# Kernel optimization log

Hardware: AMD Instinct MI355X
Metric: run time of the kernel (lower is better)

## Reference

```python
import jax, jax.numpy as jnp
import numpy as np
from jax import lax

B, C_IN, C_OUT, H, W = 2, 128, 256, 128, 128
KH = KW = 3
K = KH * KW  # 9 kernel sampling locations
EPS = 1e-5


def setup_inputs() -> dict:
    ks = jax.random.split(jax.random.key(0), 9)
    x = jax.random.normal(ks[0], (B, C_IN, H, W), dtype=jnp.float32)
    # offset/mask conv: 27 = 3*K output channels, 3x3 kernel, stride 1, same pad
    w_off = jax.random.normal(ks[1], (3 * K, C_IN, KH, KW), dtype=jnp.float32) * 0.01
    b_off = jnp.zeros((3 * K,), dtype=jnp.float32)
    # deformable conv weight [C_out, C_in, 3, 3] + bias
    w_dcn = jax.random.normal(ks[2], (C_OUT, C_IN, KH, KW), dtype=jnp.float32) * (1.0 / np.sqrt(C_IN * K))
    b_dcn = jax.random.normal(ks[3], (C_OUT,), dtype=jnp.float32) * 0.01
    # BatchNorm (inference-mode) params
    gamma = 1.0 + 0.1 * jax.random.normal(ks[4], (C_OUT,), dtype=jnp.float32)
    beta = 0.1 * jax.random.normal(ks[5], (C_OUT,), dtype=jnp.float32)
    moving_mean = 0.1 * jax.random.normal(ks[6], (C_OUT,), dtype=jnp.float32)
    moving_var = jax.random.uniform(ks[7], (C_OUT,), dtype=jnp.float32, minval=0.5, maxval=1.5)
    return {"x": x, "w_off": w_off, "b_off": b_off, "w_dcn": w_dcn, "b_dcn": b_dcn,
            "gamma": gamma, "beta": beta, "moving_mean": moving_mean, "moving_var": moving_var}


def _conv2d_nchw(x, w, b):
    y = lax.conv_general_dilated(x, w, window_strides=(1, 1), padding='SAME',
                                 dimension_numbers=('NCHW', 'OIHW', 'NCHW'))
    return y + b[None, :, None, None]


def _bilinear_gather(x, yi, xi):
    """Gather x[b,:,yi,xi] with zero padding outside. x:[B,C,H,W]; yi,xi:[B,K,H,W] int."""
    valid = ((yi >= 0) & (yi < H) & (xi >= 0) & (xi < W)).astype(x.dtype)  # [B,K,H,W]
    yc = jnp.clip(yi, 0, H - 1)
    xc = jnp.clip(xi, 0, W - 1)
    idx = (yc * W + xc).reshape(B, -1)  # [B, K*H*W]
    xf = x.reshape(B, C_IN, H * W)
    g = jax.vmap(lambda xb, ib: xb[:, ib])(xf, idx)  # [B, C, K*H*W]
    return g.reshape(B, C_IN, K, H, W) * valid[:, None]


def _deform_conv(x, offset, mask, w, b):
    """DCNv2 modulated deformable conv, 3x3, stride 1, SAME (pad=1).
    offset: [B, 2K, H, W] with (dy, dx) interleaved per kernel location (tfa/DCNv2 layout).
    mask:   [B, K, H, W] (already sigmoided).
    """
    dy = offset[:, 0::2]  # [B,K,H,W]
    dx = offset[:, 1::2]
    ky = (jnp.arange(K, dtype=jnp.float32) // KW) - 1.0  # kernel y offsets in {-1,0,1}
    kx = (jnp.arange(K, dtype=jnp.float32) % KW) - 1.0
    ii = jnp.arange(H, dtype=jnp.float32)[:, None]
    jj = jnp.arange(W, dtype=jnp.float32)[None, :]
    py = ii[None, None] + ky[None, :, None, None] + dy  # [B,K,H,W] sampling y
    px = jj[None, None] + kx[None, :, None, None] + dx  # [B,K,H,W] sampling x

    y0f = jnp.floor(py)
    x0f = jnp.floor(px)
    wy = (py - y0f)[:, None]  # [B,1,K,H,W]
    wx = (px - x0f)[:, None]
    y0 = y0f.astype(jnp.int32)
    x0 = x0f.astype(jnp.int32)

    v00 = _bilinear_gather(x, y0, x0)
    v01 = _bilinear_gather(x, y0, x0 + 1)
    v10 = _bilinear_gather(x, y0 + 1, x0)
    v11 = _bilinear_gather(x, y0 + 1, x0 + 1)
    val = (v00 * (1 - wy) * (1 - wx) + v01 * (1 - wy) * wx
           + v10 * wy * (1 - wx) + v11 * wy * wx)  # [B,C,K,H,W]
    val = val * mask[:, None]  # modulation

    w_r = w.reshape(C_OUT, C_IN, K)
    out = jnp.einsum('bckhw,ock->bohw', val, w_r)
    return out + b[None, :, None, None]


def reference(x, w_off, b_off, w_dcn, b_dcn, gamma, beta, moving_mean, moving_var):
    weight_info = _conv2d_nchw(x, w_off, b_off)  # [B, 27, H, W]
    o1, o2, m = jnp.split(weight_info, 3, axis=1)
    offset = jnp.concatenate((o1, o2), axis=1)  # [B, 18, H, W]
    mask = jax.nn.sigmoid(m)  # [B, 9, H, W]
    y = _deform_conv(x, offset, mask, w_dcn, b_dcn)
    # BatchNorm2d (inference, channels_first) + ReLU
    inv = gamma / jnp.sqrt(moving_var + EPS)
    y = (y - moving_mean[None, :, None, None]) * inv[None, :, None, None] + beta[None, :, None, None]
    return jax.nn.relu(y)
```

## Files before the change

### kernel.cpp

```cpp
#include <hip/hip_runtime.h>
#include <hip/hip_fp16.h>

#define HH 128
#define WW 128
#define CIN 128
#define COUT 256
#define K9 9
#define HW (HH*WW)
#define PIX (2*HW)
#define KDIM (CIN*K9)
#define BN_EPS 1e-5f

typedef __attribute__((ext_vector_type(8))) short short8;
typedef __attribute__((ext_vector_type(4))) float f32x4;
typedef _Float16 half8 __attribute__((ext_vector_type(8)));
typedef unsigned short u16;
typedef unsigned int u32;

union H8 { short8 s; __half2 h2[4]; half8 h; };

struct __align__(16) Meta16 { ushort4 idx; __half2 w01, w23; };
static_assert(sizeof(Meta16) == 16, "");

__device__ __forceinline__ u16 f2h(float f) {
    union { __half h; u16 u; } x; x.h = __float2half_rn(f); return x.u;
}

__global__ __launch_bounds__(256) void prep_xt(const float* __restrict__ x,
                                               u16* __restrict__ xt) {
    __shared__ float tile[32][129];
    const int b   = blockIdx.y;
    const int hw0 = blockIdx.x * 32;
    const float* __restrict__ xb = x + (size_t)b * (CIN*HW);
    #pragma unroll
    for (int i = 0; i < 16; ++i) {
        const int idx = threadIdx.x + i*256;
        const int c = idx >> 5, hwl = idx & 31;
        tile[hwl][c] = xb[(size_t)c*HW + hw0 + hwl];
    }
    __syncthreads();
    const int hwl = threadIdx.x >> 3;
    const int c0  = (threadIdx.x & 7) * 16;
    short8 s0, s1;
    #pragma unroll
    for (int j = 0; j < 8; ++j) {
        s0[j] = (short)f2h(tile[hwl][c0 + j]);
        s1[j] = (short)f2h(tile[hwl][c0 + 8 + j]);
    }
    u16* dst = xt + ((size_t)b*HW + hw0 + hwl)*CIN + c0;
    *(short8*)dst = s0;
    *(short8*)(dst + 8) = s1;
}

__global__ __launch_bounds__(128) void prep_wall(const float* __restrict__ w_dcn,
                                                 const float* __restrict__ w_off,
                                                 u16* __restrict__ wT2,
                                                 u16* __restrict__ wOffT2) {
    const int c = threadIdx.x;
    const int k = blockIdx.x;
    const int o = blockIdx.y;
    const int s = c >> 5, ch = c & 31;
    const int tt = k*4 + s;
    if (o < COUT) {
        wT2[((size_t)tt*COUT + o)*32 + ch] = f2h(w_dcn[(size_t)o*KDIM + c*K9 + k]);
    } else {
        const int j = o - COUT;
        wOffT2[((size_t)tt*32 + j)*32 + ch] =
            (j < 27) ? f2h(w_off[(size_t)j*KDIM + c*K9 + k]) : (u16)0;
    }
}

__global__ __launch_bounds__(512, 4) __attribute__((amdgpu_waves_per_eu(4, 4)))
void dcn_fused(
    const u16* __restrict__ xt, const u16* __restrict__ wT2,
    const u16* __restrict__ wOffT2, const float* __restrict__ b_off,
    const float* __restrict__ b_dcn, const float* __restrict__ gamma,
    const float* __restrict__ beta, const float* __restrict__ mmean,
    const float* __restrict__ mvar, float* __restrict__ out)
{
    __shared__ __align__(16) u16 Vs[2][64*128];
    __shared__ __align__(16) Meta16 metaL[K9*64];
    float* wiL = (float*)&Vs[0][0];

    const int t = threadIdx.x, l = t & 63, wv = t >> 6;
    const int l15 = l & 15, lq = l >> 4;
    const int bid = (blockIdx.x & 7) * 64 + (blockIdx.x >> 3);
    const int pg0 = bid * 64;
    const int b   = pg0 >> 14;
    const int hw0 = pg0 & 16383;
    const u16* __restrict__ xtb = xt + (size_t)b * (HW*CIN);

    {
        const int pxg = wv >> 1;
        const int jh  = wv & 1;
        const int px  = pxg*16 + l15;
        const int pg  = pg0 + px;
        const int hw  = pg & 16383;
        const int h = hw >> 7, w = hw & 127;
        f32x4 oa = {0.f,0.f,0.f,0.f};
        #pragma unroll
        for (int tt = 0; tt < 36; ++tt) {
            const int k = tt >> 2, c0 = (tt & 3) * 32;
            const int yy = h + (k/3) - 1, xx = w + (k%3) - 1;
            const bool valid = ((unsigned)yy < HH) && ((unsigned)xx < WW);
            const int idx = min(max(yy,0),HH-1)*WW + min(max(xx,0),WW-1);
            H8 bv, av;
            bv.s = *(const short8*)(xtb + (size_t)idx*CIN + c0 + lq*8);
            av.s = *(const short8*)(wOffT2 + ((size_t)tt*32 + jh*16 + l15)*32 + lq*8);
            if (!valid) bv.s = (short8){0,0,0,0,0,0,0,0};
            oa = __builtin_amdgcn_mfma_f32_16x16x32_f16(av.h, bv.h, oa, 0,0,0);
        }
        #pragma unroll
        for (int r = 0; r < 4; ++r)
            wiL[px*33 + jh*16 + lq*4 + r] = oa[r];
        __syncthreads();

        #pragma unroll
        for (int rd = 0; rd < 2; ++rd) {
            const int u = t + rd*512;
            if (u < 576) {
                const int px2 = u & 63, k = u >> 6;
                const int hwp = (pg0 + px2) & 16383;
                const int hp = hwp >> 7, wp = hwp & 127;
                const float dy = wiL[px2*33 + 2*k]     + b_off[2*k];
                const float dx = wiL[px2*33 + 2*k + 1] + b_off[2*k+1];
                const float mm = wiL[px2*33 + 18 + k]  + b_off[18+k];
                const float py = (float)hp + (float)(k/3) - 1.0f + dy;
                const float px_ = (float)wp + (float)(k%3) - 1.0f + dx;
                const float msk = 1.0f / (1.0f + expf(-mm));
                const float y0f = floorf(py), x0f = floorf(px_);
                const float wy = py - y0f, wx = px_ - x0f;
                const int y0 = (int)y0f, x0 = (int)x0f;
                const int y1 = y0 + 1,   x1 = x0 + 1;
                const bool v00 = ((unsigned)y0 < HH) && ((unsigned)x0 < WW);
                const bool v01 = ((unsigned)y0 < HH) && ((unsigned)x1 < WW);
                const bool v10 = ((unsigned)y1 < HH) && ((unsigned)x0 < WW);
                const bool v11 = ((unsigned)y1 < HH) && ((unsigned)x1 < WW);
                const int y0c = min(max(y0,0),HH-1), y1c = min(max(y1,0),HH-1);
                const int x0c = min(max(x0,0),WW-1), x1c = min(max(x1,0),WW-1);
                Meta16 mo;
                mo.idx.x = (u16)(y0c*WW + x0c);
                mo.idx.y = (u16)(y0c*WW + x1c);
                mo.idx.z = (u16)(y1c*WW + x0c);
                mo.idx.w = (u16)(y1c*WW + x1c);
                const float f00 = v00 ? (1.f-wy)*(1.f-wx)*msk : 0.f;
                const float f01 = v01 ? (1.f-wy)*wx*msk       : 0.f;
                const float f10 = v10 ? wy*(1.f-wx)*msk       : 0.f;
                const float f11 = v11 ? wy*wx*msk             : 0.f;
                mo.w01 = __floats2half2_rn(f00, f01);
                mo.w23 = __floats2half2_rn(f10, f11);
                metaL[k*64 + px2] = mo;
            }
        }
        __syncthreads();
    }

    const int pxl  = t >> 3;
    const int cb   = t & 7;
    const int px15 = pxl & 15;

    f32x4 acc[8];
    #pragma unroll
    for (int i = 0; i < 8; ++i) acc[i] = (f32x4){0.f,0.f,0.f,0.f};

    const u16 *g0, *g1, *g2, *g3;
    __half2 wb0, wb1, wb2, wb3;

#define SETMETA(k_) do { \
    const Meta16 mt_ = metaL[(k_)*64 + pxl]; \
    g0 = xtb + (size_t)mt_.idx.x*CIN + cb*8; \
    g1 = xtb + (size_t)mt_.idx.y*CIN + cb*8; \
    g2 = xtb + (size_t)mt_.idx.z*CIN + cb*8; \
    g3 = xtb + (size_t)mt_.idx.w*CIN + cb*8; \
    wb0 = __half2half2(__low2half(mt_.w01)); \
    wb1 = __half2half2(__high2half(mt_.w01)); \
    wb2 = __half2half2(__low2half(mt_.w23)); \
    wb3 = __half2half2(__high2half(mt_.w23)); \
} while (0)

#define ISSUE(cr_, u_) do { \
    cr_[0].s = *(const short8*)(g0 + (u_)*64); \
    cr_[1].s = *(const short8*)(g1 + (u_)*64); \
    cr_[2].s = *(const short8*)(g2 + (u_)*64); \
    cr_[3].s = *(const short8*)(g3 + (u_)*64); \
} while (0)

#define COMBINE_WRITE(cr_, u_, buf_) do { \
    H8 r_; \
    _Pragma("unroll") \
    for (int i_ = 0; i_ < 4; ++i_) \
        r_.h2[i_] = __hfma2(cr_[3].h2[i_], wb3, __hfma2(cr_[2].h2[i_], wb2, \
                    __hfma2(cr_[1].h2[i_], wb1, __hmul2(cr_[0].h2[i_], wb0)))); \
    *(short8*)&Vs[buf_][pxl*128 + ((cb + (u_)*8) ^ px15)*8] = r_.s; \
} while (0)

    H8 cA[4], cB[4];
    SETMETA(0);
    ISSUE(cA, 0); ISSUE(cB, 1);
    COMBINE_WRITE(cA, 0, 0); COMBINE_WRITE(cB, 1, 0);
    __syncthreads();

    int cur = 0;
    for (int k = 0; k < 9; ++k) {
        const bool pf = (k < 8);
        H8 av[4][2];
        #pragma unroll
        for (int s = 0; s < 4; ++s)
            #pragma unroll
            for (int m = 0; m < 2; ++m)
                av[s][m].s = *(const short8*)
                    (wT2 + ((size_t)(k*4 + s)*COUT + wv*32 + m*16 + l15)*32 + lq*8);
        __builtin_amdgcn_sched_barrier(0);
        if (pf) { SETMETA(k+1); ISSUE(cA, 0); ISSUE(cB, 1); }
        __builtin_amdgcn_sched_barrier(0);

        #pragma unroll
        for (int s = 0; s < 4; ++s) {
            #pragma unroll
            for (int nh = 0; nh < 2; ++nh) {
                H8 bf[2];
                #pragma unroll
                for (int j = 0; j < 2; ++j) {
                    const int n = nh*2 + j;
                    bf[j].s = *(const short8*)
                        &Vs[cur][(n*16 + l15)*128 + ((s*4 + lq) ^ l15)*8];
                }
                #pragma unroll
                for (int m = 0; m < 2; ++m)
                    #pragma unroll
                    for (int j = 0; j < 2; ++j)
                        acc[m*4 + nh*2 + j] =
                            __builtin_amdgcn_mfma_f32_16x16x32_f16(
                                av[s][m].h, bf[j].h, acc[m*4 + nh*2 + j], 0, 0, 0);
            }
        }
        if (pf) { COMBINE_WRITE(cA, 0, cur ^ 1); COMBINE_WRITE(cB, 1, cur ^ 1); }
        __syncthreads();
        cur ^= 1;
    }
#undef SETMETA
#undef ISSUE
#undef COMBINE_WRITE

    #pragma unroll
    for (int m = 0; m < 2; ++m) {
        #pragma unroll
        for (int r = 0; r < 4; ++r) {
            const int o = wv*32 + m*16 + lq*4 + r;
            const float sc = gamma[o] * rsqrtf(mvar[o] + BN_EPS);
            const float sh = (b_dcn[o] - mmean[o]) * sc + beta[o];
            float* __restrict__ op = out + ((size_t)(b*COUT + o) << 14) + hw0;
            #pragma unroll
            for (int n = 0; n < 4; ++n) {
                const float v = fmaf(acc[m*4 + n][r], sc, sh);
                op[n*16 + l15] = fmaxf(v, 0.f);
            }
        }
    }
}

extern "C" void kernel_launch(void* const* d_in, const int* in_sizes, int n_in,
                              void* d_out, int out_size, void* d_ws, size_t ws_size,
                              hipStream_t stream) {
    (void)in_sizes; (void)n_in; (void)out_size; (void)ws_size;
    const float* x      = (const float*)d_in[0];
    const float* w_off  = (const float*)d_in[1];
    const float* b_off  = (const float*)d_in[2];
    const float* w_dcn  = (const float*)d_in[3];
    const float* b_dcn  = (const float*)d_in[4];
    const float* gamma  = (const float*)d_in[5];
    const float* beta   = (const float*)d_in[6];
    const float* mmean  = (const float*)d_in[7];
    const float* mvar   = (const float*)d_in[8];
    float* out = (float*)d_out;

    char* ws = (char*)d_ws;
    u16* xtp    = (u16*)ws;
    u16* wT2    = (u16*)(ws + 8388608);
    u16* wOffT2 = (u16*)(ws + 8388608 + 589824);

    prep_xt  <<<dim3(HW/32, 2), 256, 0, stream>>>(x, xtp);
    prep_wall<<<dim3(9, 288), 128, 0, stream>>>(w_dcn, w_off, wT2, wOffT2);
    dcn_fused<<<dim3(PIX/64), 512, 0, stream>>>(xtp, wT2, wOffT2, b_off, b_dcn,
                                                gamma, beta, mmean, mvar, out);
}
```

Measured before the change: 73.39 us.

## Merge prep kernels and split offset-conv K loop across waves

The two preprocessing kernels (input transpose to fp16 NHWC and weight repacking) become one launch that picks its role from the block index, removing a kernel launch and the gap between launches. In the fused kernel the offset/mask conv now splits the 36-step reduction into two halves across wave groups. Each wave computes both 16-row output halves from a single B-operand load, and the two partial sums are stored in separate LDS planes and added when offsets are decoded. This halves the serial MFMA chain per wave and reuses the gathered input, at the cost of an extra LDS plane read per value.

```diff
diff --git a/kernel.cpp b/kernel.cpp
--- a/kernel.cpp
+++ b/kernel.cpp
@@ -26,47 +26,49 @@
     union { __half h; u16 u; } x; x.h = __float2half_rn(f); return x.u;
 }
 
-__global__ __launch_bounds__(256) void prep_xt(const float* __restrict__ x,
-                                               u16* __restrict__ xt) {
+__global__ __launch_bounds__(256) void prep_all(
+    const float* __restrict__ x, const float* __restrict__ w_dcn,
+    const float* __restrict__ w_off, u16* __restrict__ xt,
+    u16* __restrict__ wT2, u16* __restrict__ wOffT2)
+{
     __shared__ float tile[32][129];
-    const int b   = blockIdx.y;
-    const int hw0 = blockIdx.x * 32;
-    const float* __restrict__ xb = x + (size_t)b * (CIN*HW);
-    #pragma unroll
-    for (int i = 0; i < 16; ++i) {
-        const int idx = threadIdx.x + i*256;
-        const int c = idx >> 5, hwl = idx & 31;
-        tile[hwl][c] = xb[(size_t)c*HW + hw0 + hwl];
-    }
-    __syncthreads();
-    const int hwl = threadIdx.x >> 3;
-    const int c0  = (threadIdx.x & 7) * 16;
-    short8 s0, s1;
-    #pragma unroll
-    for (int j = 0; j < 8; ++j) {
-        s0[j] = (short)f2h(tile[hwl][c0 + j]);
-        s1[j] = (short)f2h(tile[hwl][c0 + 8 + j]);
-    }
-    u16* dst = xt + ((size_t)b*HW + hw0 + hwl)*CIN + c0;
-    *(short8*)dst = s0;
-    *(short8*)(dst + 8) = s1;
-}
-
-__global__ __launch_bounds__(128) void prep_wall(const float* __restrict__ w_dcn,
-                                                 const float* __restrict__ w_off,
-                                                 u16* __restrict__ wT2,
-                                                 u16* __restrict__ wOffT2) {
-    const int c = threadIdx.x;
-    const int k = blockIdx.x;
-    const int o = blockIdx.y;
-    const int s = c >> 5, ch = c & 31;
-    const int tt = k*4 + s;
-    if (o < COUT) {
-        wT2[((size_t)tt*COUT + o)*32 + ch] = f2h(w_dcn[(size_t)o*KDIM + c*K9 + k]);
+    if (blockIdx.x < 1024) {
+        const int b   = blockIdx.x >> 9;
+        const int hw0 = (blockIdx.x & 511) * 32;
+        const float* __restrict__ xb = x + (size_t)b * (CIN*HW);
+        #pragma unroll
+        for (int i = 0; i < 16; ++i) {
+            const int idx = threadIdx.x + i*256;
+            const int c = idx >> 5, hwl = idx & 31;
+            tile[hwl][c] = xb[(size_t)c*HW + hw0 + hwl];
+        }
+        __syncthreads();
+        const int hwl = threadIdx.x >> 3;
+        const int c0  = (threadIdx.x & 7) * 16;
+        short8 s0, s1;
+        #pragma unroll
+        for (int j = 0; j < 8; ++j) {
+            s0[j] = (short)f2h(tile[hwl][c0 + j]);
+            s1[j] = (short)f2h(tile[hwl][c0 + 8 + j]);
+        }
+        u16* dst = xt + ((size_t)b*HW + hw0 + hwl)*CIN + c0;
+        *(short8*)dst = s0;
+        *(short8*)(dst + 8) = s1;
     } else {
-        const int j = o - COUT;
-        wOffT2[((size_t)tt*32 + j)*32 + ch] =
-            (j < 27) ? f2h(w_off[(size_t)j*KDIM + c*K9 + k]) : (u16)0;
+        const int u2 = (blockIdx.x - 1024) * 2 + (threadIdx.x >> 7);
+        const int c  = threadIdx.x & 127;
+        const int k  = u2 % 9;
+        const int o  = u2 / 9;
+        const int s = c >> 5, ch = c & 31;
+        const int tt = k*4 + s;
+        if (o < COUT) {
+            wT2[((size_t)tt*COUT + o)*32 + ch] =
+                f2h(w_dcn[(size_t)o*KDIM + c*K9 + k]);
+        } else {
+            const int j = o - COUT;
+            wOffT2[((size_t)tt*32 + j)*32 + ch] =
+                (j < 27) ? f2h(w_off[(size_t)j*KDIM + c*K9 + k]) : (u16)0;
+        }
     }
 }
 
@@ -80,7 +82,6 @@
 {
     __shared__ __align__(16) u16 Vs[2][64*128];
     __shared__ __align__(16) Meta16 metaL[K9*64];
-    float* wiL = (float*)&Vs[0][0];
 
     const int t = threadIdx.x, l = t & 63, wv = t >> 6;
     const int l15 = l & 15, lq = l >> 4;
@@ -91,30 +92,38 @@
     const u16* __restrict__ xtb = xt + (size_t)b * (HW*CIN);
 
     {
-        const int pxg = wv >> 1;
-        const int jh  = wv & 1;
+        const int pxg = wv & 3;
+        const int ks  = wv >> 2;
         const int px  = pxg*16 + l15;
         const int pg  = pg0 + px;
         const int hw  = pg & 16383;
         const int h = hw >> 7, w = hw & 127;
-        f32x4 oa = {0.f,0.f,0.f,0.f};
-        #pragma unroll
-        for (int tt = 0; tt < 36; ++tt) {
+        f32x4 oa0 = {0.f,0.f,0.f,0.f}, oa1 = {0.f,0.f,0.f,0.f};
+        #pragma unroll
+        for (int it = 0; it < 18; ++it) {
+            const int tt = ks*18 + it;
             const int k = tt >> 2, c0 = (tt & 3) * 32;
             const int yy = h + (k/3) - 1, xx = w + (k%3) - 1;
             const bool valid = ((unsigned)yy < HH) && ((unsigned)xx < WW);
             const int idx = min(max(yy,0),HH-1)*WW + min(max(xx,0),WW-1);
-            H8 bv, av;
+            H8 bv, a0, a1;
             bv.s = *(const short8*)(xtb + (size_t)idx*CIN + c0 + lq*8);
-            av.s = *(const short8*)(wOffT2 + ((size_t)tt*32 + jh*16 + l15)*32 + lq*8);
+            a0.s = *(const short8*)(wOffT2 + ((size_t)tt*32 + l15)*32      + lq*8);
+            a1.s = *(const short8*)(wOffT2 + ((size_t)tt*32 + 16 + l15)*32 + lq*8);
             if (!valid) bv.s = (short8){0,0,0,0,0,0,0,0};
-            oa = __builtin_amdgcn_mfma_f32_16x16x32_f16(av.h, bv.h, oa, 0,0,0);
-        }
-        #pragma unroll
-        for (int r = 0; r < 4; ++r)
-            wiL[px*33 + jh*16 + lq*4 + r] = oa[r];
-        __syncthreads();
-
+            oa0 = __builtin_amdgcn_mfma_f32_16x16x32_f16(a0.h, bv.h, oa0, 0,0,0);
+            oa1 = __builtin_amdgcn_mfma_f32_16x16x32_f16(a1.h, bv.h, oa1, 0,0,0);
+        }
+        float* plane = (float*)&Vs[ks][0];
+        #pragma unroll
+        for (int r = 0; r < 4; ++r) {
+            plane[px*33 + lq*4 + r]      = oa0[r];
+            plane[px*33 + 16 + lq*4 + r] = oa1[r];
+        }
+        __syncthreads();
+
+        const float* __restrict__ p0 = (const float*)&Vs[0][0];
+        const float* __restrict__ p1 = (const float*)&Vs[1][0];
         #pragma unroll
         for (int rd = 0; rd < 2; ++rd) {
             const int u = t + rd*512;
@@ -122,9 +131,9 @@
                 const int px2 = u & 63, k = u >> 6;
                 const int hwp = (pg0 + px2) & 16383;
                 const int hp = hwp >> 7, wp = hwp & 127;
-                const float dy = wiL[px2*33 + 2*k]     + b_off[2*k];
-                const float dx = wiL[px2*33 + 2*k + 1] + b_off[2*k+1];
-                const float mm = wiL[px2*33 + 18 + k]  + b_off[18+k];
+                const float dy = p0[px2*33 + 2*k]     + p1[px2*33 + 2*k]     + b_off[2*k];
+                const float dx = p0[px2*33 + 2*k + 1] + p1[px2*33 + 2*k + 1] + b_off[2*k+1];
+                const float mm = p0[px2*33 + 18 + k]  + p1[px2*33 + 18 + k]  + b_off[18+k];
                 const float py = (float)hp + (float)(k/3) - 1.0f + dy;
                 const float px_ = (float)wp + (float)(k%3) - 1.0f + dx;
                 const float msk = 1.0f / (1.0f + expf(-mm));
@@ -279,8 +288,8 @@
     u16* wT2    = (u16*)(ws + 8388608);
     u16* wOffT2 = (u16*)(ws + 8388608 + 589824);
 
-    prep_xt  <<<dim3(HW/32, 2), 256, 0, stream>>>(x, xtp);
-    prep_wall<<<dim3(9, 288), 128, 0, stream>>>(w_dcn, w_off, wT2, wOffT2);
+    prep_all <<<dim3(1024 + 1296), 256, 0, stream>>>(x, w_dcn, w_off,
+                                                     xtp, wT2, wOffT2);
     dcn_fused<<<dim3(PIX/64), 512, 0, stream>>>(xtp, wT2, wOffT2, b_off, b_dcn,
                                                 gamma, beta, mmean, mvar, out);
 }
```

New measurement: 64.04 us (median of 2 runs). 12.7% less time.
